# Optimization experiments

Measured on AMD Instinct MI355X. Metric: run time of the kernel, lower is better.

The kernel has to match this reference:

```python
import jax, jax.numpy as jnp
import numpy as np

EMBED = 1024
HEADS = 16
HEAD_DIM = EMBED // HEADS
FF = 4096
LN_EPS = 1e-5


def _layer_norm(x, scale, bias):
    mu = jnp.mean(x, axis=-1, keepdims=True)
    var = jnp.mean(jnp.square(x - mu), axis=-1, keepdims=True)
    return (x - mu) * jax.lax.rsqrt(var + LN_EPS) * scale + bias


def setup_inputs() -> dict:
    key = jax.random.key(0)
    ks = jax.random.split(key, 16)
    B, T, CARRY = 8, 128, 4096
    s = 0.02
    return {
        "hidden": jax.random.normal(ks[0], (B, T, EMBED), jnp.float32),
        "key_carry": jax.random.normal(ks[1], (B, HEADS, CARRY, HEAD_DIM), jnp.float32),
        "value_carry": jax.random.normal(ks[2], (B, HEADS, CARRY, HEAD_DIM), jnp.float32),
        "ln1_scale": jnp.ones((EMBED,), jnp.float32),
        "ln1_bias": jnp.zeros((EMBED,), jnp.float32),
        "wq": jax.random.normal(ks[3], (EMBED, EMBED), jnp.float32) * s,
        "bq": jnp.zeros((EMBED,), jnp.float32),
        "wk": jax.random.normal(ks[4], (EMBED, EMBED), jnp.float32) * s,
        "bk": jnp.zeros((EMBED,), jnp.float32),
        "wv": jax.random.normal(ks[5], (EMBED, EMBED), jnp.float32) * s,
        "bv": jnp.zeros((EMBED,), jnp.float32),
        "wo": jax.random.normal(ks[6], (EMBED, EMBED), jnp.float32) * s,
        "bo": jnp.zeros((EMBED,), jnp.float32),
        "ln2_scale": jnp.ones((EMBED,), jnp.float32),
        "ln2_bias": jnp.zeros((EMBED,), jnp.float32),
        "w1": jax.random.normal(ks[7], (EMBED, FF), jnp.float32) * s,
        "b1": jnp.zeros((FF,), jnp.float32),
        "w2": jax.random.normal(ks[8], (FF, EMBED), jnp.float32) * s,
        "b2": jnp.zeros((EMBED,), jnp.float32),
    }


def reference(hidden, key_carry, value_carry, ln1_scale, ln1_bias, wq, bq, wk, bk,
              wv, bv, wo, bo, ln2_scale, ln2_bias, w1, b1, w2, b2):
    B, T, _ = hidden.shape
    carry_len = key_carry.shape[2]

    x = _layer_norm(hidden, ln1_scale, ln1_bias)
    # [B, H, T, Dh]
    def split_heads(y):
        return y.reshape(B, T, HEADS, HEAD_DIM).transpose(0, 2, 1, 3)
    q = split_heads(x @ wq + bq)
    k = split_heads(x @ wk + bk)
    v = split_heads(x @ wv + bv)

    k_all = jnp.concatenate([key_carry, k], axis=2)   # [B,H,C+T,Dh]
    v_all = jnp.concatenate([value_carry, v], axis=2)

    scores = jnp.einsum("bhtd,bhsd->bhts", q, k_all) / jnp.sqrt(jnp.float32(HEAD_DIM))
    kv_pos = jnp.arange(carry_len + T)
    q_pos = jnp.arange(T)[:, None] + carry_len
    causal = kv_pos[None, :] <= q_pos  # [T, C+T]
    scores = jnp.where(causal[None, None], scores, jnp.float32(-jnp.inf))
    attn = jax.nn.softmax(scores, axis=-1)  # dropout=0.0 (eval)
    ctx = jnp.einsum("bhts,bhsd->bhtd", attn, v_all)
    ctx = ctx.transpose(0, 2, 1, 3).reshape(B, T, EMBED)
    hidden = hidden + (ctx @ wo + bo)

    f = _layer_norm(hidden, ln2_scale, ln2_bias)
    f = jax.nn.gelu(f @ w1 + b1, approximate=False) @ w2 + b2
    hidden = hidden + f
    return hidden, k_all, v_all
```

## Files before the change

kernel.cpp:

```cpp
#include <hip/hip_runtime.h>
#include <hip/hip_bf16.h>
#include <math.h>

#define EMBED 1024
#define HEADS 16
#define HDIM 64
#define FFDIM 4096
#define BATCH 8
#define TLEN 128
#define CARRY 4096
#define SEQA (CARRY + TLEN)
#define MROWS (BATCH * TLEN)
#define NSPLIT 8

typedef __attribute__((ext_vector_type(8))) short bf16x8;
typedef __attribute__((ext_vector_type(4))) float f32x4;
typedef unsigned short u16;

static __device__ __forceinline__ u16 f2b(float v) {
    __hip_bfloat16 h = __float2bfloat16(v);
    return *reinterpret_cast<u16*>(&h);
}

typedef const __attribute__((address_space(1))) unsigned int g_u32;
typedef __attribute__((address_space(3))) unsigned int l_u32;
static __device__ __forceinline__ void gl16(const void* g, void* l) {
    __builtin_amdgcn_global_load_lds((g_u32*)g, (l_u32*)l, 16, 0, 0);
}

static __device__ __forceinline__ void bar_lgkm() {
    asm volatile("s_waitcnt lgkmcnt(0)" ::: "memory");
    __builtin_amdgcn_s_barrier();
    __builtin_amdgcn_sched_barrier(0);
}
static __device__ __forceinline__ void bar_plain() {
    __builtin_amdgcn_sched_barrier(0);
    __builtin_amdgcn_s_barrier();
}

__global__ void copy_carry_kernel(const float4* __restrict__ kc, const float4* __restrict__ vc,
                                  float4* __restrict__ k_all, float4* __restrict__ v_all) {
    const size_t total = (size_t)BATCH * HEADS * CARRY * HDIM / 4;
    const size_t DH = (size_t)SEQA * HDIM / 4;
    for (size_t e = (size_t)blockIdx.x * blockDim.x + threadIdx.x; e < total;
         e += (size_t)gridDim.x * blockDim.x) {
        size_t bh = e >> 16;
        size_t rem = e & 65535;
        size_t d = bh * DH + rem;
        k_all[d] = kc[e];
        v_all[d] = vc[e];
    }
}

__global__ __launch_bounds__(256) void ln_kernel(const float* __restrict__ in,
                                                 const float* __restrict__ scale,
                                                 const float* __restrict__ bias,
                                                 u16* __restrict__ out) {
    int row = blockIdx.x;
    int tid = threadIdx.x;
    const float4* rin = (const float4*)(in + (size_t)row * EMBED);
    float4 v = rin[tid];
    float s = v.x + v.y + v.z + v.w;
    float s2 = v.x * v.x + v.y * v.y + v.z * v.z + v.w * v.w;
    for (int o = 32; o > 0; o >>= 1) {
        s += __shfl_down(s, o, 64);
        s2 += __shfl_down(s2, o, 64);
    }
    __shared__ float ls[8], ls2[8];
    int wid = tid >> 6, lane = tid & 63;
    if (lane == 0) { ls[wid] = s; ls2[wid] = s2; }
    __syncthreads();
    if (tid == 0) {
        float S = 0.f, S2 = 0.f;
        for (int i = 0; i < 4; i++) { S += ls[i]; S2 += ls2[i]; }
        float mu = S * (1.0f / EMBED);
        float var = S2 * (1.0f / EMBED) - mu * mu;
        ls[0] = mu;
        ls2[0] = rsqrtf(var + 1e-5f);
    }
    __syncthreads();
    float mu = ls[0], rstd = ls2[0];
    float sc[4], bi[4], xin[4];
    *(float4*)sc = ((const float4*)scale)[tid];
    *(float4*)bi = ((const float4*)bias)[tid];
    *(float4*)xin = v;
    u16 o0 = f2b((xin[0] - mu) * rstd * sc[0] + bi[0]);
    u16 o1 = f2b((xin[1] - mu) * rstd * sc[1] + bi[1]);
    u16 o2 = f2b((xin[2] - mu) * rstd * sc[2] + bi[2]);
    u16 o3 = f2b((xin[3] - mu) * rstd * sc[3] + bi[3]);
    unsigned int u0 = (unsigned int)o0 | ((unsigned int)o1 << 16);
    unsigned int u1 = (unsigned int)o2 | ((unsigned int)o3 << 16);
    uint2 pk = {u0, u1};
    *(uint2*)(out + (size_t)row * EMBED + tid * 4) = pk;
}

__global__ __launch_bounds__(256) void transpose_all(const float* __restrict__ wq,
                                                     const float* __restrict__ wk,
                                                     const float* __restrict__ wv,
                                                     const float* __restrict__ wo,
                                                     const float* __restrict__ w1,
                                                     const float* __restrict__ w2,
                                                     const float* __restrict__ bq,
                                                     const float* __restrict__ bk,
                                                     const float* __restrict__ bv,
                                                     u16* __restrict__ wqkvT,
                                                     u16* __restrict__ woT,
                                                     u16* __restrict__ w1T,
                                                     u16* __restrict__ w2T,
                                                     float* __restrict__ bias_qkv) {
    __shared__ float Ls[64][65];
    int z = blockIdx.z;
    int bx = blockIdx.x, by = blockIdx.y;
    const float* W;
    u16* WT;
    int K, N;
    if (z < 4) {
        W = (z == 0) ? wq : (z == 1) ? wk : (z == 2) ? wv : wo;
        WT = (z < 3) ? (wqkvT + (size_t)z * 1024 * 1024) : woT;
        K = 1024; N = 1024;
    } else if (z < 8) {
        W = w1; WT = w1T; K = 1024; N = 4096; bx += (z - 4) * 16;
    } else {
        W = w2; WT = w2T; K = 4096; N = 1024; by += (z - 8) * 16;
    }
    int tid = threadIdx.x;
    if (z == 3 && blockIdx.y == 0 && blockIdx.x < 12) {
        int i = blockIdx.x * 256 + tid;
        bias_qkv[i] = (i < 1024) ? bq[i] : (i < 2048) ? bk[i - 1024] : bv[i - 2048];
    }
    int k0 = by * 64, n0 = bx * 64;
#pragma unroll
    for (int p = 0; p < 4; p++) {
        int r = (tid >> 4) + 16 * p, c = (tid & 15) * 4;
        float4 v = *(const float4*)(W + (size_t)(k0 + r) * N + n0 + c);
        Ls[r][c] = v.x; Ls[r][c + 1] = v.y; Ls[r][c + 2] = v.z; Ls[r][c + 3] = v.w;
    }
    __syncthreads();
#pragma unroll
    for (int p = 0; p < 4; p++) {
        int n = (tid >> 4) + 16 * p, k4 = (tid & 15) * 4;
        u16 o0 = f2b(Ls[k4][n]), o1 = f2b(Ls[k4 + 1][n]);
        u16 o2 = f2b(Ls[k4 + 2][n]), o3 = f2b(Ls[k4 + 3][n]);
        unsigned int a = (unsigned int)o0 | ((unsigned int)o1 << 16);
        unsigned int b = (unsigned int)o2 | ((unsigned int)o3 << 16);
        uint2 pk = {a, b};
        *(uint2*)(WT + (size_t)(n0 + n) * K + k0 + k4) = pk;
    }
}

static __device__ __forceinline__ void stage2(const u16* __restrict__ Ag,
                                              const u16* __restrict__ Wg,
                                              u16* As, u16* Ws,
                                              int w, int l, int K) {
    int r0 = 16 * w + (l >> 3);
    int scol = ((l & 7) ^ (l >> 3)) * 8;
    char* a0 = (char*)As + w * 2048;
    char* w0 = (char*)Ws + w * 2048;
    gl16(Ag + (size_t)r0 * K + scol, a0);
    gl16(Ag + (size_t)(r0 + 8) * K + scol, a0 + 1024);
    gl16(Wg + (size_t)r0 * K + scol, w0);
    gl16(Wg + (size_t)(r0 + 8) * K + scol, w0 + 1024);
}

template <int MODE>
__global__ __launch_bounds__(256) void gemm_bf16(const u16* __restrict__ A,
                                                 const u16* __restrict__ WT,
                                                 const float* __restrict__ bias,
                                                 const float* __restrict__ resid,
                                                 float* __restrict__ outf,
                                                 float* __restrict__ outf2,
                                                 u16* __restrict__ outb, int N, int K) {
    __shared__ u16 As[64 * 64];
    __shared__ u16 Ws[64 * 64];
    int tid = threadIdx.x;
    int m0 = blockIdx.y * 64, n0 = blockIdx.x * 64;
    int w = tid >> 6, l = tid & 63, lr = l & 15, lg = l >> 4;
    f32x4 acc[4] = {};

    const u16* Ag = A + (size_t)m0 * K;
    const u16* Wg = WT + (size_t)n0 * K;

    for (int k0 = 0; k0 < K; k0 += 64) {
        __syncthreads();
        stage2(Ag + k0, Wg + k0, As, Ws, w, l, K);
        __syncthreads();
#pragma unroll
        for (int ks = 0; ks < 2; ks++) {
            int abyte = ((16 * w + lr) * 128 + lg * 16 + ks * 64) ^ ((lr & 7) << 4);
            bf16x8 af = *(bf16x8*)((char*)As + abyte);
#pragma unroll
            for (int f = 0; f < 4; f++) {
                int bbyte = ((16 * f + lr) * 128 + lg * 16 + ks * 64) ^ ((lr & 7) << 4);
                bf16x8 bfr = *(bf16x8*)((char*)Ws + bbyte);
                acc[f] = __builtin_amdgcn_mfma_f32_16x16x32_bf16(af, bfr, acc[f], 0, 0, 0);
            }
        }
    }

    int gr0 = m0 + 16 * w + 4 * lg;
#pragma unroll
    for (int f = 0; f < 4; f++) {
        int gc = n0 + 16 * f + lr;
        float bv = bias[gc];
#pragma unroll
        for (int r = 0; r < 4; r++) {
            int gm = gr0 + r;
            float v = acc[f][r] + bv;
            if (MODE == 3) v = 0.5f * v * (1.0f + erff(v * 0.70710678118654752f));
            if (MODE == 2 || MODE == 4) v += resid[(size_t)gm * EMBED + gc];
            if (MODE == 0 || MODE == 3) {
                outb[(size_t)gm * N + gc] = f2b(v);
            } else if (MODE == 1) {
                int b_ = gm >> 7, t_ = gm & 127, h_ = gc >> 6, d_ = gc & 63;
                outf[(((size_t)(b_ * HEADS + h_)) * SEQA + CARRY + t_) * HDIM + d_] = v;
            } else if (MODE == 5) {
                if (gc < 1024) {
                    outb[(size_t)gm * EMBED + gc] = f2b(v);
                } else {
                    int which = gc >> 10;
                    int gc2 = gc & 1023;
                    int b_ = gm >> 7, t_ = gm & 127, h_ = gc2 >> 6, d_ = gc2 & 63;
                    float* dst = (which == 1) ? outf : outf2;
                    dst[(((size_t)(b_ * HEADS + h_)) * SEQA + CARRY + t_) * HDIM + d_] = v;
                }
            } else {
                outf[(size_t)gm * EMBED + gc] = v;
            }
        }
    }
}

__global__ __launch_bounds__(256) void gemm_splitk(const u16* __restrict__ A,
                                                   const u16* __restrict__ WT,
                                                   float* __restrict__ part,
                                                   int N, int Ktot, int Klen) {
    __shared__ u16 As[64 * 64];
    __shared__ u16 Ws[64 * 64];
    int tid = threadIdx.x;
    int m0 = blockIdx.y * 64, n0 = blockIdx.x * 64;
    int k0s = blockIdx.z * Klen;
    int w = tid >> 6, l = tid & 63, lr = l & 15, lg = l >> 4;
    f32x4 acc[4] = {};

    const u16* Ag = A + (size_t)m0 * Ktot;
    const u16* Wg = WT + (size_t)n0 * Ktot;

    for (int k0 = k0s; k0 < k0s + Klen; k0 += 64) {
        __syncthreads();
        stage2(Ag + k0, Wg + k0, As, Ws, w, l, Ktot);
        __syncthreads();
#pragma unroll
        for (int ks = 0; ks < 2; ks++) {
            int abyte = ((16 * w + lr) * 128 + lg * 16 + ks * 64) ^ ((lr & 7) << 4);
            bf16x8 af = *(bf16x8*)((char*)As + abyte);
#pragma unroll
            for (int f = 0; f < 4; f++) {
                int bbyte = ((16 * f + lr) * 128 + lg * 16 + ks * 64) ^ ((lr & 7) << 4);
                bf16x8 bfr = *(bf16x8*)((char*)Ws + bbyte);
                acc[f] = __builtin_amdgcn_mfma_f32_16x16x32_bf16(af, bfr, acc[f], 0, 0, 0);
            }
        }
    }

    float* pbase = part + (size_t)blockIdx.z * MROWS * N;
    int gr0 = m0 + 16 * w + 4 * lg;
#pragma unroll
    for (int f = 0; f < 4; f++) {
        int gc = n0 + 16 * f + lr;
#pragma unroll
        for (int r = 0; r < 4; r++)
            pbase[(size_t)(gr0 + r) * N + gc] = acc[f][r];
    }
}

template <int NS>
__global__ __launch_bounds__(256) void combine_add(const float* __restrict__ part,
                                                   const float* __restrict__ bias,
                                                   const float* __restrict__ resid,
                                                   float* __restrict__ out) {
    size_t e = ((size_t)blockIdx.x * 256 + threadIdx.x) * 4;
    int n0 = (int)(e & 1023);
    float4 v = *(const float4*)(resid + e);
    float4 b = *(const float4*)(bias + n0);
    v.x += b.x; v.y += b.y; v.z += b.z; v.w += b.w;
#pragma unroll
    for (int s = 0; s < NS; s++) {
        float4 p = *(const float4*)(part + (size_t)s * MROWS * EMBED + e);
        v.x += p.x; v.y += p.y; v.z += p.z; v.w += p.w;
    }
    *(float4*)(out + e) = v;
}

__global__ __launch_bounds__(256) void combine_ln(const float* __restrict__ part,
                                                  const float* __restrict__ bias,
                                                  const float* __restrict__ resid,
                                                  const float* __restrict__ ln_s,
                                                  const float* __restrict__ ln_b,
                                                  float* __restrict__ out,
                                                  u16* __restrict__ outb) {
    int row = blockIdx.x, tid = threadIdx.x;
    size_t base = (size_t)row * EMBED + tid * 4;
    float4 v = *(const float4*)(resid + base);
    float4 b = *(const float4*)(bias + tid * 4);
    v.x += b.x; v.y += b.y; v.z += b.z; v.w += b.w;
#pragma unroll
    for (int s = 0; s < 2; s++) {
        float4 p = *(const float4*)(part + (size_t)s * MROWS * EMBED + base);
        v.x += p.x; v.y += p.y; v.z += p.z; v.w += p.w;
    }
    *(float4*)(out + base) = v;

    float s1 = v.x + v.y + v.z + v.w;
    float s2 = v.x * v.x + v.y * v.y + v.z * v.z + v.w * v.w;
    for (int o = 32; o > 0; o >>= 1) {
        s1 += __shfl_down(s1, o, 64);
        s2 += __shfl_down(s2, o, 64);
    }
    __shared__ float ls[8], ls2[8];
    int wid = tid >> 6, lane = tid & 63;
    if (lane == 0) { ls[wid] = s1; ls2[wid] = s2; }
    __syncthreads();
    if (tid == 0) {
        float S = 0.f, S2 = 0.f;
        for (int i = 0; i < 4; i++) { S += ls[i]; S2 += ls2[i]; }
        float mu = S * (1.0f / EMBED);
        float var = S2 * (1.0f / EMBED) - mu * mu;
        ls[0] = mu;
        ls2[0] = rsqrtf(var + 1e-5f);
    }
    __syncthreads();
    float mu = ls[0], rstd = ls2[0];
    float sc[4], bi[4];
    *(float4*)sc = ((const float4*)ln_s)[tid];
    *(float4*)bi = ((const float4*)ln_b)[tid];
    u16 o0 = f2b((v.x - mu) * rstd * sc[0] + bi[0]);
    u16 o1 = f2b((v.y - mu) * rstd * sc[1] + bi[1]);
    u16 o2 = f2b((v.z - mu) * rstd * sc[2] + bi[2]);
    u16 o3 = f2b((v.w - mu) * rstd * sc[3] + bi[3]);
    unsigned int u0 = (unsigned int)o0 | ((unsigned int)o1 << 16);
    unsigned int u1 = (unsigned int)o2 | ((unsigned int)o3 << 16);
    uint2 pk = {u0, u1};
    *(uint2*)(outb + base) = pk;
}

__global__ __launch_bounds__(256) void attn_mfma_split(const u16* __restrict__ qb,
                                                       const float* __restrict__ kc,
                                                       const float* __restrict__ vc,
                                                       float* __restrict__ k_all,
                                                       float* __restrict__ v_all,
                                                       float* __restrict__ part_acc,
                                                       float* __restrict__ part_m,
                                                       float* __restrict__ part_l) {
    __shared__ u16 Ks[64 * 64];
    __shared__ u16 Vt[64 * 64];
    __shared__ u16 Ps[128 * 64];

    int bh = blockIdx.x, b = bh >> 4, h = bh & 15;
    int sp = blockIdx.y;
    int tid = threadIdx.x;
    int w = tid >> 6, l = tid & 63, lr = l & 15, lg = l >> 4;

    bf16x8 qf[2][2];
#pragma unroll
    for (int rr = 0; rr < 2; rr++) {
        const u16* qrow = qb + (size_t)(b * TLEN + 32 * w + 16 * rr + lr) * EMBED + h * HDIM;
        qf[rr][0] = *(const bf16x8*)(qrow + 8 * lg);
        qf[rr][1] = *(const bf16x8*)(qrow + 8 * lg + 32);
    }

    const float* kcb = kc + (size_t)bh * CARRY * HDIM;
    const float* vcb = vc + (size_t)bh * CARRY * HDIM;
    const float* kb = k_all + (size_t)bh * SEQA * HDIM;
    const float* vb = v_all + (size_t)bh * SEQA * HDIM;
    float* kwr = k_all + (size_t)bh * SEQA * HDIM;
    float* vwr = v_all + (size_t)bh * SEQA * HDIM;

    float m_run[2][4], l_run[2][4];
    f32x4 oacc[2][4] = {};
#pragma unroll
    for (int rr = 0; rr < 2; rr++)
#pragma unroll
        for (int r = 0; r < 4; r++) { m_run[rr][r] = -1e30f; l_run[rr][r] = 0.f; }

    const int nt = SEQA / 64;
    const int tps = (nt + NSPLIT - 1) / NSPLIT;
    int kt0 = sp * tps;
    int kt1 = min(kt0 + tps, nt);

    int krow = tid >> 4;
    int vrow4 = (tid >> 4) * 4;
    int col = (tid & 15) * 4;

    float4 kA[4], vA[4], kB[4], vB[4];

    {
        bool cn = kt0 < 64;
        const float* ksrc = cn ? kcb : kb;
        const float* vsrc = cn ? vcb : vb;
#pragma unroll
        for (int p = 0; p < 4; p++)
            kA[p] = *(const float4*)(ksrc + (size_t)(kt0 * 64 + krow + 16 * p) * HDIM + col);
#pragma unroll
        for (int p = 0; p < 4; p++)
            vA[p] = *(const float4*)(vsrc + (size_t)(kt0 * 64 + vrow4 + p) * HDIM + col);
    }

    auto body = [&](float4 (&kc_)[4], float4 (&vc_)[4],
                    float4 (&kn_)[4], float4 (&vn_)[4], int kt) {
        bool carry_t = kt < 64;
        int ktn = kt + 1;
        if (ktn < kt1) {
            bool cn = ktn < 64;
            const float* ksrc = cn ? kcb : kb;
            const float* vsrc = cn ? vcb : vb;
#pragma unroll
            for (int p = 0; p < 4; p++)
                kn_[p] = *(const float4*)(ksrc + (size_t)(ktn * 64 + krow + 16 * p) * HDIM + col);
#pragma unroll
            for (int p = 0; p < 4; p++)
                vn_[p] = *(const float4*)(vsrc + (size_t)(ktn * 64 + vrow4 + p) * HDIM + col);
        }
        if (carry_t) {
#pragma unroll
            for (int p = 0; p < 4; p++)
                *(float4*)(kwr + (size_t)(kt * 64 + krow + 16 * p) * HDIM + col) = kc_[p];
#pragma unroll
            for (int p = 0; p < 4; p++)
                *(float4*)(vwr + (size_t)(kt * 64 + vrow4 + p) * HDIM + col) = vc_[p];
        }
        bar_plain();
#pragma unroll
        for (int p = 0; p < 4; p++) {
            int s = krow + 16 * p;
            u16 t0 = f2b(kc_[p].x), t1 = f2b(kc_[p].y), t2 = f2b(kc_[p].z), t3 = f2b(kc_[p].w);
            unsigned int a = (unsigned int)t0 | ((unsigned int)t1 << 16);
            unsigned int bq = (unsigned int)t2 | ((unsigned int)t3 << 16);
            uint2 pk = {a, bq};
            *(uint2*)((char*)Ks + ((s * 128 + col * 2) ^ ((s & 7) << 4))) = pk;
        }
#pragma unroll
        for (int i = 0; i < 4; i++) {
            int d = col + i;
            u16 e0 = f2b(((const float*)&vc_[0])[i]);
            u16 e1 = f2b(((const float*)&vc_[1])[i]);
            u16 e2 = f2b(((const float*)&vc_[2])[i]);
            u16 e3 = f2b(((const float*)&vc_[3])[i]);
            unsigned int a = (unsigned int)e0 | ((unsigned int)e1 << 16);
            unsigned int bq = (unsigned int)e2 | ((unsigned int)e3 << 16);
            uint2 pk = {a, bq};
            *(uint2*)((char*)Vt + ((d * 128 + vrow4 * 2) ^ ((d & 7) << 4))) = pk;
        }
        bar_lgkm();

#pragma unroll
        for (int rr = 0; rr < 2; rr++) {
            float x[4][4];
#pragma unroll
            for (int f = 0; f < 4; f++) {
                int row = 16 * f + lr;
                int swz = (row & 7) << 4;
                bf16x8 kf0 = *(bf16x8*)((char*)Ks + ((row * 128 + 16 * lg) ^ swz));
                bf16x8 kf1 = *(bf16x8*)((char*)Ks + ((row * 128 + 16 * lg + 64) ^ swz));
                f32x4 z = {};
                z = __builtin_amdgcn_mfma_f32_16x16x32_bf16(qf[rr][0], kf0, z, 0, 0, 0);
                z = __builtin_amdgcn_mfma_f32_16x16x32_bf16(qf[rr][1], kf1, z, 0, 0, 0);
#pragma unroll
                for (int r = 0; r < 4; r++) x[f][r] = z[r] * 0.125f;
            }
            if (kt * 64 + 63 > CARRY + 32 * w + 16 * rr) {
#pragma unroll
                for (int f = 0; f < 4; f++) {
                    int sg = kt * 64 + 16 * f + lr;
#pragma unroll
                    for (int r = 0; r < 4; r++) {
                        int tg = 32 * w + 16 * rr + 4 * lg + r;
                        if (sg > CARRY + tg) x[f][r] = -1e30f;
                    }
                }
            }
#pragma unroll
            for (int r = 0; r < 4; r++) {
                float mt = fmaxf(fmaxf(x[0][r], x[1][r]), fmaxf(x[2][r], x[3][r]));
                mt = fmaxf(mt, __shfl_xor(mt, 1, 64));
                mt = fmaxf(mt, __shfl_xor(mt, 2, 64));
                mt = fmaxf(mt, __shfl_xor(mt, 4, 64));
                mt = fmaxf(mt, __shfl_xor(mt, 8, 64));
                float mn = fmaxf(m_run[rr][r], mt);
                float fs = __expf(m_run[rr][r] - mn);
                m_run[rr][r] = mn;
                float s = 0.f;
#pragma unroll
                for (int f = 0; f < 4; f++) {
                    float p = __expf(x[f][r] - mn);
                    x[f][r] = p;
                    s += p;
                }
                s += __shfl_xor(s, 1, 64);
                s += __shfl_xor(s, 2, 64);
                s += __shfl_xor(s, 4, 64);
                s += __shfl_xor(s, 8, 64);
                l_run[rr][r] = l_run[rr][r] * fs + s;
#pragma unroll
                for (int f2 = 0; f2 < 4; f2++) oacc[rr][f2][r] *= fs;
            }
#pragma unroll
            for (int f = 0; f < 4; f++) {
#pragma unroll
                for (int r = 0; r < 4; r++) {
                    int row = 32 * w + 16 * rr + 4 * lg + r;
                    int byte = (row * 128 + (16 * f + lr) * 2) ^ ((row & 7) << 4);
                    *(u16*)((char*)Ps + byte) = f2b(x[f][r]);
                }
            }
        }
#pragma unroll
        for (int rr = 0; rr < 2; rr++) {
            int prow = 32 * w + 16 * rr + lr;
            int pswz = (prow & 7) << 4;
            bf16x8 pa0 = *(bf16x8*)((char*)Ps + ((prow * 128 + 16 * lg) ^ pswz));
            bf16x8 pa1 = *(bf16x8*)((char*)Ps + ((prow * 128 + 16 * lg + 64) ^ pswz));
#pragma unroll
            for (int f2 = 0; f2 < 4; f2++) {
                int d = 16 * f2 + lr;
                int vswz = (d & 7) << 4;
                bf16x8 vf0 = *(bf16x8*)((char*)Vt + ((d * 128 + 16 * lg) ^ vswz));
                bf16x8 vf1 = *(bf16x8*)((char*)Vt + ((d * 128 + 16 * lg + 64) ^ vswz));
                oacc[rr][f2] = __builtin_amdgcn_mfma_f32_16x16x32_bf16(pa0, vf0, oacc[rr][f2], 0, 0, 0);
                oacc[rr][f2] = __builtin_amdgcn_mfma_f32_16x16x32_bf16(pa1, vf1, oacc[rr][f2], 0, 0, 0);
            }
        }
    };

    for (int kt = kt0; kt < kt1; kt += 2) {
        body(kA, vA, kB, vB, kt);
        if (kt + 1 < kt1) body(kB, vB, kA, vA, kt + 1);
    }

    int p = bh * NSPLIT + sp;
#pragma unroll
    for (int rr = 0; rr < 2; rr++) {
        if (lr == 0) {
#pragma unroll
            for (int r = 0; r < 4; r++) {
                int row = 32 * w + 16 * rr + 4 * lg + r;
                part_m[(size_t)p * 128 + row] = m_run[rr][r];
                part_l[(size_t)p * 128 + row] = l_run[rr][r];
            }
        }
#pragma unroll
        for (int f2 = 0; f2 < 4; f2++) {
#pragma unroll
            for (int r = 0; r < 4; r++) {
                int row = 32 * w + 16 * rr + 4 * lg + r;
                part_acc[(size_t)p * 8192 + row * 64 + 16 * f2 + lr] = oacc[rr][f2][r];
            }
        }
    }
}

__global__ __launch_bounds__(256) void attn_combine(const float* __restrict__ part_acc,
                                                    const float* __restrict__ part_m,
                                                    const float* __restrict__ part_l,
                                                    u16* __restrict__ ctx) {
    int g = blockIdx.x;
    int bh = g >> 1, qh = g & 1, b = bh >> 4, h = bh & 15;
    int t = threadIdx.x;
    int r = t >> 2, c0 = (t & 3) * 16;
    int row = qh * 64 + r;
    int p0 = bh * NSPLIT;

    float ms[NSPLIT];
    float M = -1e30f;
#pragma unroll
    for (int s = 0; s < NSPLIT; s++) {
        ms[s] = part_m[(size_t)(p0 + s) * 128 + row];
        M = fmaxf(M, ms[s]);
    }
    float wgt[NSPLIT];
    float L = 0.f;
#pragma unroll
    for (int s = 0; s < NSPLIT; s++) {
        wgt[s] = __expf(ms[s] - M);
        L += wgt[s] * part_l[(size_t)(p0 + s) * 128 + row];
    }
    float inv = 1.0f / L;

    size_t grow = (size_t)(b * TLEN + row) * EMBED + h * HDIM + c0;
#pragma unroll
    for (int j = 0; j < 16; j += 4) {
        float4 a = {0.f, 0.f, 0.f, 0.f};
#pragma unroll
        for (int s = 0; s < NSPLIT; s++) {
            float4 p = *(const float4*)(part_acc + (size_t)(p0 + s) * 8192 + row * 64 + c0 + j);
            a.x += wgt[s] * p.x; a.y += wgt[s] * p.y; a.z += wgt[s] * p.z; a.w += wgt[s] * p.w;
        }
        u16 o0 = f2b(a.x * inv), o1 = f2b(a.y * inv), o2 = f2b(a.z * inv), o3 = f2b(a.w * inv);
        unsigned int u0 = (unsigned int)o0 | ((unsigned int)o1 << 16);
        unsigned int u1 = (unsigned int)o2 | ((unsigned int)o3 << 16);
        uint2 pk = {u0, u1};
        *(uint2*)(ctx + grow + j) = pk;
    }
}

__global__ __launch_bounds__(256) void attn_mfma(const u16* __restrict__ qb,
                                                 const float* __restrict__ k_all,
                                                 const float* __restrict__ v_all,
                                                 u16* __restrict__ ctx) {
    __shared__ u16 Ks[64 * 64];
    __shared__ u16 Vt[64 * 64];
    __shared__ u16 Ps[64 * 64];

    int bh = blockIdx.x, b = bh >> 4, h = bh & 15;
    int q0 = blockIdx.y * 64;
    int tid = threadIdx.x;
    int w = tid >> 6, l = tid & 63, lr = l & 15, lg = l >> 4;

    bf16x8 qf0, qf1;
    {
        const u16* qrow = qb + (size_t)(b * TLEN + q0 + 16 * w + lr) * EMBED + h * HDIM;
        qf0 = *(const bf16x8*)(qrow + 8 * lg);
        qf1 = *(const bf16x8*)(qrow + 8 * lg + 32);
    }
    const float* kb = k_all + (size_t)bh * SEQA * HDIM;
    const float* vb = v_all + (size_t)bh * SEQA * HDIM;

    float m_run[4], l_run[4];
    f32x4 oacc[4] = {};
#pragma unroll
    for (int r = 0; r < 4; r++) { m_run[r] = -1e30f; l_run[r] = 0.f; }

    int nt = (CARRY + q0 + 64) >> 6;
    for (int kt = 0; kt < nt; kt++) {
        __syncthreads();
#pragma unroll
        for (int p = 0; p < 4; p++) {
            int s = (tid >> 4) + 16 * p, c = (tid & 15) * 4;
            float4 kv = *(const float4*)(kb + (size_t)(kt * 64 + s) * HDIM + c);
            u16 t0 = f2b(kv.x), t1 = f2b(kv.y), t2 = f2b(kv.z), t3 = f2b(kv.w);
            unsigned int a = (unsigned int)t0 | ((unsigned int)t1 << 16);
            unsigned int bq = (unsigned int)t2 | ((unsigned int)t3 << 16);
            uint2 pk = {a, bq};
            int byte = (s * 128 + c * 2) ^ ((s & 7) << 4);
            *(uint2*)((char*)Ks + byte) = pk;
        }
        {
            int d = tid & 63;
            u16 tmp[16];
#pragma unroll
            for (int q = 0; q < 16; q++)
                tmp[q] = f2b(vb[(size_t)(kt * 64 + 16 * w + q) * HDIM + d]);
            int b0 = (d * 128 + 32 * w) ^ ((d & 7) << 4);
            int b1 = (d * 128 + 32 * w + 16) ^ ((d & 7) << 4);
            *(bf16x8*)((char*)Vt + b0) = *(bf16x8*)&tmp[0];
            *(bf16x8*)((char*)Vt + b1) = *(bf16x8*)&tmp[8];
        }
        __syncthreads();

        float x[4][4];
#pragma unroll
        for (int f = 0; f < 4; f++) {
            int row = 16 * f + lr;
            int swz = (row & 7) << 4;
            bf16x8 kf0 = *(bf16x8*)((char*)Ks + ((row * 128 + 16 * lg) ^ swz));
            bf16x8 kf1 = *(bf16x8*)((char*)Ks + ((row * 128 + 16 * lg + 64) ^ swz));
            f32x4 z = {};
            z = __builtin_amdgcn_mfma_f32_16x16x32_bf16(qf0, kf0, z, 0, 0, 0);
            z = __builtin_amdgcn_mfma_f32_16x16x32_bf16(qf1, kf1, z, 0, 0, 0);
#pragma unroll
            for (int r = 0; r < 4; r++) x[f][r] = z[r] * 0.125f;
        }
        if (kt * 64 + 63 > CARRY + q0 + 16 * w) {
#pragma unroll
            for (int f = 0; f < 4; f++) {
                int sg = kt * 64 + 16 * f + lr;
#pragma unroll
                for (int r = 0; r < 4; r++) {
                    int tg = q0 + 16 * w + 4 * lg + r;
                    if (sg > CARRY + tg) x[f][r] = -1e30f;
                }
            }
        }
#pragma unroll
        for (int r = 0; r < 4; r++) {
            float mt = fmaxf(fmaxf(x[0][r], x[1][r]), fmaxf(x[2][r], x[3][r]));
            mt = fmaxf(mt, __shfl_xor(mt, 1, 64));
            mt = fmaxf(mt, __shfl_xor(mt, 2, 64));
            mt = fmaxf(mt, __shfl_xor(mt, 4, 64));
            mt = fmaxf(mt, __shfl_xor(mt, 8, 64));
            float mn = fmaxf(m_run[r], mt);
            float fs = __expf(m_run[r] - mn);
            m_run[r] = mn;
            float s = 0.f;
#pragma unroll
            for (int f = 0; f < 4; f++) {
                float p = __expf(x[f][r] - mn);
                x[f][r] = p;
                s += p;
            }
            s += __shfl_xor(s, 1, 64);
            s += __shfl_xor(s, 2, 64);
            s += __shfl_xor(s, 4, 64);
            s += __shfl_xor(s, 8, 64);
            l_run[r] = l_run[r] * fs + s;
#pragma unroll
            for (int f2 = 0; f2 < 4; f2++) oacc[f2][r] *= fs;
        }
#pragma unroll
        for (int f = 0; f < 4; f++) {
#pragma unroll
            for (int r = 0; r < 4; r++) {
                int row = 16 * w + 4 * lg + r;
                int byte = (row * 128 + (16 * f + lr) * 2) ^ ((row & 7) << 4);
                *(u16*)((char*)Ps + byte) = f2b(x[f][r]);
            }
        }
        {
            int prow = 16 * w + lr;
            int pswz = (prow & 7) << 4;
            bf16x8 pa0 = *(bf16x8*)((char*)Ps + ((prow * 128 + 16 * lg) ^ pswz));
            bf16x8 pa1 = *(bf16x8*)((char*)Ps + ((prow * 128 + 16 * lg + 64) ^ pswz));
#pragma unroll
            for (int f2 = 0; f2 < 4; f2++) {
                int d = 16 * f2 + lr;
                int vswz = (d & 7) << 4;
                bf16x8 vf0 = *(bf16x8*)((char*)Vt + ((d * 128 + 16 * lg) ^ vswz));
                bf16x8 vf1 = *(bf16x8*)((char*)Vt + ((d * 128 + 16 * lg + 64) ^ vswz));
                oacc[f2] = __builtin_amdgcn_mfma_f32_16x16x32_bf16(pa0, vf0, oacc[f2], 0, 0, 0);
                oacc[f2] = __builtin_amdgcn_mfma_f32_16x16x32_bf16(pa1, vf1, oacc[f2], 0, 0, 0);
            }
        }
    }
#pragma unroll
    for (int r = 0; r < 4; r++) {
        float inv = 1.0f / l_run[r];
        size_t grow = (size_t)(b * TLEN + q0 + 16 * w + 4 * lg + r) * EMBED + h * HDIM;
#pragma unroll
        for (int f2 = 0; f2 < 4; f2++)
            ctx[grow + 16 * f2 + lr] = f2b(oacc[f2][r] * inv);
    }
}

extern "C" void kernel_launch(void* const* d_in, const int* in_sizes, int n_in,
                              void* d_out, int out_size, void* d_ws, size_t ws_size,
                              hipStream_t stream) {
    const float* hidden = (const float*)d_in[0];
    const float* key_carry = (const float*)d_in[1];
    const float* value_carry = (const float*)d_in[2];
    const float* ln1_s = (const float*)d_in[3];
    const float* ln1_b = (const float*)d_in[4];
    const float* wq = (const float*)d_in[5];
    const float* bq = (const float*)d_in[6];
    const float* wk = (const float*)d_in[7];
    const float* bk = (const float*)d_in[8];
    const float* wv = (const float*)d_in[9];
    const float* bv = (const float*)d_in[10];
    const float* wo = (const float*)d_in[11];
    const float* bo = (const float*)d_in[12];
    const float* ln2_s = (const float*)d_in[13];
    const float* ln2_b = (const float*)d_in[14];
    const float* w1 = (const float*)d_in[15];
    const float* b1 = (const float*)d_in[16];
    const float* w2 = (const float*)d_in[17];
    const float* b2 = (const float*)d_in[18];

    float* out_hidden = (float*)d_out;
    float* k_all = out_hidden + (size_t)MROWS * EMBED;
    float* v_all = k_all + (size_t)BATCH * HEADS * SEQA * HDIM;

    u16* wsu = (u16*)d_ws;
    u16* wqkvT = wsu;
    u16* woT = wsu + 3145728;
    u16* w1T = wsu + 4194304;
    u16* w2T = wsu + 8388608;
    u16* xb  = wsu + 12582912;
    u16* qbb = wsu + 13631488;
    u16* ctxb = wsu + 14680064;
    u16* fb  = wsu + 15728640;
    u16* h1b = wsu + 16777216;
    float* bias_qkv = (float*)(wsu + 20971520);
    float* part = (float*)(wsu + 20977664);
    const size_t nparts = (size_t)128 * NSPLIT;
    const size_t need = (size_t)20977664 * 2 +
                        (nparts * 8192 + 2 * nparts * 128) * 4;

    transpose_all<<<dim3(16, 16, 12), 256, 0, stream>>>(wq, wk, wv, wo, w1, w2, bq, bk, bv,
                                                        wqkvT, woT, w1T, w2T, bias_qkv);

    ln_kernel<<<MROWS, 256, 0, stream>>>(hidden, ln1_s, ln1_b, xb);

    if (ws_size >= need) {
        gemm_bf16<5><<<dim3(48, 16), 256, 0, stream>>>(xb, wqkvT, bias_qkv, nullptr,
                                                       k_all, v_all, qbb, 3072, EMBED);
        float* part_acc = part;
        float* part_m = part + nparts * 8192;
        float* part_l = part_m + nparts * 128;
        attn_mfma_split<<<dim3(BATCH * HEADS, NSPLIT), 256, 0, stream>>>(
            qbb, key_carry, value_carry, k_all, v_all, part_acc, part_m, part_l);
        attn_combine<<<256, 256, 0, stream>>>(part_acc, part_m, part_l, ctxb);

        gemm_splitk<<<dim3(16, 16, 2), 256, 0, stream>>>(ctxb, woT, part, EMBED, EMBED, 512);
        combine_ln<<<1024, 256, 0, stream>>>(part, bo, hidden, ln2_s, ln2_b, out_hidden, fb);

        gemm_bf16<3><<<dim3(64, 16), 256, 0, stream>>>(fb, w1T, b1, nullptr, nullptr, nullptr,
                                                       h1b, FFDIM, EMBED);
        gemm_splitk<<<dim3(16, 16, 4), 256, 0, stream>>>(h1b, w2T, part, EMBED, FFDIM, 1024);
        combine_add<4><<<1024, 256, 0, stream>>>(part, b2, out_hidden, out_hidden);
    } else {
        copy_carry_kernel<<<2048, 256, 0, stream>>>(
            (const float4*)key_carry, (const float4*)value_carry,
            (float4*)k_all, (float4*)v_all);
        u16* wqT = wqkvT;
        u16* wkT = wqkvT + 1048576;
        u16* wvT = wqkvT + 2097152;
        gemm_bf16<0><<<dim3(16, 16), 256, 0, stream>>>(xb, wqT, bq, nullptr, nullptr, nullptr,
                                                       qbb, EMBED, EMBED);
        gemm_bf16<1><<<dim3(16, 16), 256, 0, stream>>>(xb, wkT, bk, nullptr, k_all, nullptr,
                                                       nullptr, EMBED, EMBED);
        gemm_bf16<1><<<dim3(16, 16), 256, 0, stream>>>(xb, wvT, bv, nullptr, v_all, nullptr,
                                                       nullptr, EMBED, EMBED);
        attn_mfma<<<dim3(BATCH * HEADS, 2), 256, 0, stream>>>(qbb, k_all, v_all, ctxb);
        gemm_bf16<2><<<dim3(16, 16), 256, 0, stream>>>(ctxb, woT, bo, hidden, out_hidden,
                                                       nullptr, nullptr, EMBED, EMBED);
        ln_kernel<<<MROWS, 256, 0, stream>>>(out_hidden, ln2_s, ln2_b, fb);
        gemm_bf16<3><<<dim3(64, 16), 256, 0, stream>>>(fb, w1T, b1, nullptr, nullptr, nullptr,
                                                       h1b, FFDIM, EMBED);
        gemm_bf16<4><<<dim3(16, 16), 256, 0, stream>>>(h1b, w2T, b2, out_hidden, out_hidden,
                                                       nullptr, nullptr, EMBED, FFDIM);
    }
}
```

Measured before the change: 289.0 us.

## Restructure split attention softmax with lazy rescale and MFMA row sums

Folds the 1/sqrt(d) score scale into the Q projection epilogue. The attention kernel now skips the running-max update unless some score exceeds the current max by more than a threshold, which is the lazy rescale used in FlashAttention-style kernels. Row sums are computed with an MFMA against a ones vector instead of cross-lane shuffles. Query rows are reassigned so the P tile in LDS is halved and reused per query half, and the two-stage register double buffer is replaced by a single prefetch buffer. The trade-offs are an extra barrier-ordered LDS reuse pattern, bf16 rounding of P inside the row sum, and a possibly less overlapped load pipeline.

```diff
diff --git a/kernel.cpp b/kernel.cpp
--- a/kernel.cpp
+++ b/kernel.cpp
@@ -215,7 +215,7 @@
                 outf[(((size_t)(b_ * HEADS + h_)) * SEQA + CARRY + t_) * HDIM + d_] = v;
             } else if (MODE == 5) {
                 if (gc < 1024) {
-                    outb[(size_t)gm * EMBED + gc] = f2b(v);
+                    outb[(size_t)gm * EMBED + gc] = f2b(v * 0.125f);
                 } else {
                     int which = gc >> 10;
                     int gc2 = gc & 1023;
@@ -353,7 +353,7 @@
                                                        float* __restrict__ part_l) {
     __shared__ u16 Ks[64 * 64];
     __shared__ u16 Vt[64 * 64];
-    __shared__ u16 Ps[128 * 64];
+    __shared__ u16 Ps[64 * 64];
 
     int bh = blockIdx.x, b = bh >> 4, h = bh & 15;
     int sp = blockIdx.y;
@@ -362,11 +362,15 @@
 
     bf16x8 qf[2][2];
 #pragma unroll
-    for (int rr = 0; rr < 2; rr++) {
-        const u16* qrow = qb + (size_t)(b * TLEN + 32 * w + 16 * rr + lr) * EMBED + h * HDIM;
-        qf[rr][0] = *(const bf16x8*)(qrow + 8 * lg);
-        qf[rr][1] = *(const bf16x8*)(qrow + 8 * lg + 32);
-    }
+    for (int qh = 0; qh < 2; qh++) {
+        const u16* qrow = qb + (size_t)(b * TLEN + qh * 64 + 16 * w + lr) * EMBED + h * HDIM;
+        qf[qh][0] = *(const bf16x8*)(qrow + 8 * lg);
+        qf[qh][1] = *(const bf16x8*)(qrow + 8 * lg + 32);
+    }
+
+    bf16x8 onesf;
+#pragma unroll
+    for (int j = 0; j < 8; j++) onesf[j] = (short)0x3F80;
 
     const float* kcb = kc + (size_t)bh * CARRY * HDIM;
     const float* vcb = vc + (size_t)bh * CARRY * HDIM;
@@ -375,12 +379,13 @@
     float* kwr = k_all + (size_t)bh * SEQA * HDIM;
     float* vwr = v_all + (size_t)bh * SEQA * HDIM;
 
-    float m_run[2][4], l_run[2][4];
+    float m_run[2][4];
+    f32x4 lacc[2] = {};
     f32x4 oacc[2][4] = {};
 #pragma unroll
-    for (int rr = 0; rr < 2; rr++)
-#pragma unroll
-        for (int r = 0; r < 4; r++) { m_run[rr][r] = -1e30f; l_run[rr][r] = 0.f; }
+    for (int qh = 0; qh < 2; qh++)
+#pragma unroll
+        for (int r = 0; r < 4; r++) m_run[qh][r] = -1e30f;
 
     const int nt = SEQA / 64;
     const int tps = (nt + NSPLIT - 1) / NSPLIT;
@@ -391,7 +396,7 @@
     int vrow4 = (tid >> 4) * 4;
     int col = (tid & 15) * 4;
 
-    float4 kA[4], vA[4], kB[4], vB[4];
+    float4 kr[4], vr[4];
 
     {
         bool cn = kt0 < 64;
@@ -399,15 +404,44 @@
         const float* vsrc = cn ? vcb : vb;
 #pragma unroll
         for (int p = 0; p < 4; p++)
-            kA[p] = *(const float4*)(ksrc + (size_t)(kt0 * 64 + krow + 16 * p) * HDIM + col);
+            kr[p] = *(const float4*)(ksrc + (size_t)(kt0 * 64 + krow + 16 * p) * HDIM + col);
 #pragma unroll
         for (int p = 0; p < 4; p++)
-            vA[p] = *(const float4*)(vsrc + (size_t)(kt0 * 64 + vrow4 + p) * HDIM + col);
-    }
-
-    auto body = [&](float4 (&kc_)[4], float4 (&vc_)[4],
-                    float4 (&kn_)[4], float4 (&vn_)[4], int kt) {
+            vr[p] = *(const float4*)(vsrc + (size_t)(kt0 * 64 + vrow4 + p) * HDIM + col);
+    }
+
+    for (int kt = kt0; kt < kt1; kt++) {
         bool carry_t = kt < 64;
+        bar_plain();
+#pragma unroll
+        for (int p = 0; p < 4; p++) {
+            int s = krow + 16 * p;
+            u16 t0 = f2b(kr[p].x), t1 = f2b(kr[p].y), t2 = f2b(kr[p].z), t3 = f2b(kr[p].w);
+            unsigned int a = (unsigned int)t0 | ((unsigned int)t1 << 16);
+            unsigned int bq = (unsigned int)t2 | ((unsigned int)t3 << 16);
+            uint2 pk = {a, bq};
+            *(uint2*)((char*)Ks + ((s * 128 + col * 2) ^ ((s & 7) << 4))) = pk;
+        }
+#pragma unroll
+        for (int i = 0; i < 4; i++) {
+            int d = col + i;
+            u16 e0 = f2b(((const float*)&vr[0])[i]);
+            u16 e1 = f2b(((const float*)&vr[1])[i]);
+            u16 e2 = f2b(((const float*)&vr[2])[i]);
+            u16 e3 = f2b(((const float*)&vr[3])[i]);
+            unsigned int a = (unsigned int)e0 | ((unsigned int)e1 << 16);
+            unsigned int bq = (unsigned int)e2 | ((unsigned int)e3 << 16);
+            uint2 pk = {a, bq};
+            *(uint2*)((char*)Vt + ((d * 128 + vrow4 * 2) ^ ((d & 7) << 4))) = pk;
+        }
+        if (carry_t) {
+#pragma unroll
+            for (int p = 0; p < 4; p++)
+                *(float4*)(kwr + (size_t)(kt * 64 + krow + 16 * p) * HDIM + col) = kr[p];
+#pragma unroll
+            for (int p = 0; p < 4; p++)
+                *(float4*)(vwr + (size_t)(kt * 64 + vrow4 + p) * HDIM + col) = vr[p];
+        }
         int ktn = kt + 1;
         if (ktn < kt1) {
             bool cn = ktn < 64;
@@ -415,45 +449,16 @@
             const float* vsrc = cn ? vcb : vb;
 #pragma unroll
             for (int p = 0; p < 4; p++)
-                kn_[p] = *(const float4*)(ksrc + (size_t)(ktn * 64 + krow + 16 * p) * HDIM + col);
+                kr[p] = *(const float4*)(ksrc + (size_t)(ktn * 64 + krow + 16 * p) * HDIM + col);
 #pragma unroll
             for (int p = 0; p < 4; p++)
-                vn_[p] = *(const float4*)(vsrc + (size_t)(ktn * 64 + vrow4 + p) * HDIM + col);
-        }
-        if (carry_t) {
-#pragma unroll
-            for (int p = 0; p < 4; p++)
-                *(float4*)(kwr + (size_t)(kt * 64 + krow + 16 * p) * HDIM + col) = kc_[p];
-#pragma unroll
-            for (int p = 0; p < 4; p++)
-                *(float4*)(vwr + (size_t)(kt * 64 + vrow4 + p) * HDIM + col) = vc_[p];
-        }
-        bar_plain();
-#pragma unroll
-        for (int p = 0; p < 4; p++) {
-            int s = krow + 16 * p;
-            u16 t0 = f2b(kc_[p].x), t1 = f2b(kc_[p].y), t2 = f2b(kc_[p].z), t3 = f2b(kc_[p].w);
-            unsigned int a = (unsigned int)t0 | ((unsigned int)t1 << 16);
-            unsigned int bq = (unsigned int)t2 | ((unsigned int)t3 << 16);
-            uint2 pk = {a, bq};
-            *(uint2*)((char*)Ks + ((s * 128 + col * 2) ^ ((s & 7) << 4))) = pk;
-        }
-#pragma unroll
-        for (int i = 0; i < 4; i++) {
-            int d = col + i;
-            u16 e0 = f2b(((const float*)&vc_[0])[i]);
-            u16 e1 = f2b(((const float*)&vc_[1])[i]);
-            u16 e2 = f2b(((const float*)&vc_[2])[i]);
-            u16 e3 = f2b(((const float*)&vc_[3])[i]);
-            unsigned int a = (unsigned int)e0 | ((unsigned int)e1 << 16);
-            unsigned int bq = (unsigned int)e2 | ((unsigned int)e3 << 16);
-            uint2 pk = {a, bq};
-            *(uint2*)((char*)Vt + ((d * 128 + vrow4 * 2) ^ ((d & 7) << 4))) = pk;
+                vr[p] = *(const float4*)(vsrc + (size_t)(ktn * 64 + vrow4 + p) * HDIM + col);
         }
         bar_lgkm();
 
 #pragma unroll
-        for (int rr = 0; rr < 2; rr++) {
+        for (int qh = 0; qh < 2; qh++) {
+            int q0 = qh * 64;
             float x[4][4];
 #pragma unroll
             for (int f = 0; f < 4; f++) {
@@ -462,97 +467,95 @@
                 bf16x8 kf0 = *(bf16x8*)((char*)Ks + ((row * 128 + 16 * lg) ^ swz));
                 bf16x8 kf1 = *(bf16x8*)((char*)Ks + ((row * 128 + 16 * lg + 64) ^ swz));
                 f32x4 z = {};
-                z = __builtin_amdgcn_mfma_f32_16x16x32_bf16(qf[rr][0], kf0, z, 0, 0, 0);
-                z = __builtin_amdgcn_mfma_f32_16x16x32_bf16(qf[rr][1], kf1, z, 0, 0, 0);
-#pragma unroll
-                for (int r = 0; r < 4; r++) x[f][r] = z[r] * 0.125f;
-            }
-            if (kt * 64 + 63 > CARRY + 32 * w + 16 * rr) {
+                z = __builtin_amdgcn_mfma_f32_16x16x32_bf16(qf[qh][0], kf0, z, 0, 0, 0);
+                z = __builtin_amdgcn_mfma_f32_16x16x32_bf16(qf[qh][1], kf1, z, 0, 0, 0);
+#pragma unroll
+                for (int r = 0; r < 4; r++) x[f][r] = z[r];
+            }
+            if (kt * 64 + 63 > CARRY + q0 + 16 * w) {
 #pragma unroll
                 for (int f = 0; f < 4; f++) {
                     int sg = kt * 64 + 16 * f + lr;
 #pragma unroll
                     for (int r = 0; r < 4; r++) {
-                        int tg = 32 * w + 16 * rr + 4 * lg + r;
+                        int tg = q0 + 16 * w + 4 * lg + r;
                         if (sg > CARRY + tg) x[f][r] = -1e30f;
                     }
                 }
             }
-#pragma unroll
-            for (int r = 0; r < 4; r++) {
-                float mt = fmaxf(fmaxf(x[0][r], x[1][r]), fmaxf(x[2][r], x[3][r]));
-                mt = fmaxf(mt, __shfl_xor(mt, 1, 64));
-                mt = fmaxf(mt, __shfl_xor(mt, 2, 64));
-                mt = fmaxf(mt, __shfl_xor(mt, 4, 64));
-                mt = fmaxf(mt, __shfl_xor(mt, 8, 64));
-                float mn = fmaxf(m_run[rr][r], mt);
-                float fs = __expf(m_run[rr][r] - mn);
-                m_run[rr][r] = mn;
-                float s = 0.f;
-#pragma unroll
-                for (int f = 0; f < 4; f++) {
-                    float p = __expf(x[f][r] - mn);
-                    x[f][r] = p;
-                    s += p;
+            float lm[4];
+#pragma unroll
+            for (int r = 0; r < 4; r++)
+                lm[r] = fmaxf(fmaxf(x[0][r], x[1][r]), fmaxf(x[2][r], x[3][r]));
+            bool need = __any(lm[0] > m_run[qh][0] + 8.f) || __any(lm[1] > m_run[qh][1] + 8.f) ||
+                        __any(lm[2] > m_run[qh][2] + 8.f) || __any(lm[3] > m_run[qh][3] + 8.f);
+            if (need) {
+#pragma unroll
+                for (int r = 0; r < 4; r++) {
+                    float mt = lm[r];
+                    mt = fmaxf(mt, __shfl_xor(mt, 1, 64));
+                    mt = fmaxf(mt, __shfl_xor(mt, 2, 64));
+                    mt = fmaxf(mt, __shfl_xor(mt, 4, 64));
+                    mt = fmaxf(mt, __shfl_xor(mt, 8, 64));
+                    float mn = fmaxf(m_run[qh][r], mt);
+                    float fs = __expf(m_run[qh][r] - mn);
+                    m_run[qh][r] = mn;
+                    lacc[qh][r] *= fs;
+#pragma unroll
+                    for (int f2 = 0; f2 < 4; f2++) oacc[qh][f2][r] *= fs;
                 }
-                s += __shfl_xor(s, 1, 64);
-                s += __shfl_xor(s, 2, 64);
-                s += __shfl_xor(s, 4, 64);
-                s += __shfl_xor(s, 8, 64);
-                l_run[rr][r] = l_run[rr][r] * fs + s;
-#pragma unroll
-                for (int f2 = 0; f2 < 4; f2++) oacc[rr][f2][r] *= fs;
-            }
+            }
+#pragma unroll
+            for (int f = 0; f < 4; f++)
+#pragma unroll
+                for (int r = 0; r < 4; r++)
+                    x[f][r] = __expf(x[f][r] - m_run[qh][r]);
 #pragma unroll
             for (int f = 0; f < 4; f++) {
 #pragma unroll
                 for (int r = 0; r < 4; r++) {
-                    int row = 32 * w + 16 * rr + 4 * lg + r;
+                    int row = 16 * w + 4 * lg + r;
                     int byte = (row * 128 + (16 * f + lr) * 2) ^ ((row & 7) << 4);
                     *(u16*)((char*)Ps + byte) = f2b(x[f][r]);
                 }
             }
-        }
-#pragma unroll
-        for (int rr = 0; rr < 2; rr++) {
-            int prow = 32 * w + 16 * rr + lr;
-            int pswz = (prow & 7) << 4;
-            bf16x8 pa0 = *(bf16x8*)((char*)Ps + ((prow * 128 + 16 * lg) ^ pswz));
-            bf16x8 pa1 = *(bf16x8*)((char*)Ps + ((prow * 128 + 16 * lg + 64) ^ pswz));
-#pragma unroll
-            for (int f2 = 0; f2 < 4; f2++) {
-                int d = 16 * f2 + lr;
-                int vswz = (d & 7) << 4;
-                bf16x8 vf0 = *(bf16x8*)((char*)Vt + ((d * 128 + 16 * lg) ^ vswz));
-                bf16x8 vf1 = *(bf16x8*)((char*)Vt + ((d * 128 + 16 * lg + 64) ^ vswz));
-                oacc[rr][f2] = __builtin_amdgcn_mfma_f32_16x16x32_bf16(pa0, vf0, oacc[rr][f2], 0, 0, 0);
-                oacc[rr][f2] = __builtin_amdgcn_mfma_f32_16x16x32_bf16(pa1, vf1, oacc[rr][f2], 0, 0, 0);
-            }
-        }
-    };
-
-    for (int kt = kt0; kt < kt1; kt += 2) {
-        body(kA, vA, kB, vB, kt);
-        if (kt + 1 < kt1) body(kB, vB, kA, vA, kt + 1);
+            {
+                int prow = 16 * w + lr;
+                int pswz = (prow & 7) << 4;
+                bf16x8 pa0 = *(bf16x8*)((char*)Ps + ((prow * 128 + 16 * lg) ^ pswz));
+                bf16x8 pa1 = *(bf16x8*)((char*)Ps + ((prow * 128 + 16 * lg + 64) ^ pswz));
+                lacc[qh] = __builtin_amdgcn_mfma_f32_16x16x32_bf16(pa0, onesf, lacc[qh], 0, 0, 0);
+                lacc[qh] = __builtin_amdgcn_mfma_f32_16x16x32_bf16(pa1, onesf, lacc[qh], 0, 0, 0);
+#pragma unroll
+                for (int f2 = 0; f2 < 4; f2++) {
+                    int d = 16 * f2 + lr;
+                    int vswz = (d & 7) << 4;
+                    bf16x8 vf0 = *(bf16x8*)((char*)Vt + ((d * 128 + 16 * lg) ^ vswz));
+                    bf16x8 vf1 = *(bf16x8*)((char*)Vt + ((d * 128 + 16 * lg + 64) ^ vswz));
+                    oacc[qh][f2] = __builtin_amdgcn_mfma_f32_16x16x32_bf16(pa0, vf0, oacc[qh][f2], 0, 0, 0);
+                    oacc[qh][f2] = __builtin_amdgcn_mfma_f32_16x16x32_bf16(pa1, vf1, oacc[qh][f2], 0, 0, 0);
+                }
+            }
+        }
     }
 
     int p = bh * NSPLIT + sp;
 #pragma unroll
-    for (int rr = 0; rr < 2; rr++) {
+    for (int qh = 0; qh < 2; qh++) {
         if (lr == 0) {
 #pragma unroll
             for (int r = 0; r < 4; r++) {
-                int row = 32 * w + 16 * rr + 4 * lg + r;
-                part_m[(size_t)p * 128 + row] = m_run[rr][r];
-                part_l[(size_t)p * 128 + row] = l_run[rr][r];
+                int row = qh * 64 + 16 * w + 4 * lg + r;
+                part_m[(size_t)p * 128 + row] = m_run[qh][r];
+                part_l[(size_t)p * 128 + row] = lacc[qh][r];
             }
         }
 #pragma unroll
         for (int f2 = 0; f2 < 4; f2++) {
 #pragma unroll
             for (int r = 0; r < 4; r++) {
-                int row = 32 * w + 16 * rr + 4 * lg + r;
-                part_acc[(size_t)p * 8192 + row * 64 + 16 * f2 + lr] = oacc[rr][f2][r];
+                int row = qh * 64 + 16 * w + 4 * lg + r;
+                part_acc[(size_t)p * 8192 + row * 64 + 16 * f2 + lr] = oacc[qh][f2][r];
             }
         }
     }
```

Result: faster. 237.4 us (median of 2 runs) (-17.8%).
